# Performance work log

Hardware: AMD Instinct MI355X
Metric: run time of the kernel (lower is better)

The kernel has to match this reference:

```python
import jax, jax.numpy as jnp
import numpy as np


def conv1d_same(x, w, b, dilation=1):
    # x: [B, T, Cin], w: [K, Cin, Cout] (WIO), 'same' padding, stride 1
    y = jax.lax.conv_general_dilated(
        x, w, window_strides=(1,), padding='SAME',
        rhs_dilation=(dilation,), dimension_numbers=('NWC', 'WIO', 'NWC'))
    return y + b


def setup_inputs() -> dict:
    key = jax.random.key(0)
    ks = jax.random.split(key, 6)
    B, T, N_IN, N_OUT, ATTN_DIM, KSZ = 16, 2048, 96, 128, 64, 3
    return {
        'x': jax.random.normal(ks[0], (B, T, N_IN), jnp.float32),
        'qkv_w': jax.random.normal(ks[1], (N_IN, 3 * ATTN_DIM), jnp.float32) * 0.05,
        'qkv_b': jnp.zeros((3 * ATTN_DIM,), jnp.float32),
        'scale': jnp.ones((), jnp.float32),
        'conv_w1': jax.random.normal(ks[2], (KSZ, ATTN_DIM, N_OUT), jnp.float32) * 0.05,
        'conv_b1': jnp.zeros((N_OUT,), jnp.float32),
        'conv_w2': jax.random.normal(ks[3], (KSZ, N_OUT, N_OUT), jnp.float32) * 0.05,
        'conv_b2': jnp.zeros((N_OUT,), jnp.float32),
        'down_w': jax.random.normal(ks[4], (N_IN, N_OUT), jnp.float32) * 0.1,
    }


def reference(x, qkv_w, qkv_b, scale, conv_w1, conv_b1, conv_w2, conv_b2, down_w):
    # Dense4Attention: single Dense(3*attn_dim), split into q,k,v
    qkv = x @ qkv_w + qkv_b                       # [B,T,3*D]
    q, k, v = jnp.split(qkv, 3, axis=-1)          # each [B,T,D]
    # AttentionBlock: scores = q k^T * learned scale; non-causal (default)
    scores = jnp.einsum('btd,bsd->bts', q, k) * scale   # [B,T,T]
    weights = jax.nn.softmax(scores, axis=2)            # softmax_axis=2
    out_attn = jnp.einsum('bts,bsd->btd', weights, v)   # [B,T,D]
    h = jax.nn.relu(conv1d_same(out_attn, conv_w1, conv_b1, 1))
    out = jax.nn.relu(conv1d_same(h, conv_w2, conv_b2, 1))   # [B,T,n_out]
    # enhanced residual: softmax over time of row-sums of attn weights
    weight_x = jax.nn.softmax(jnp.sum(weights, axis=2), axis=1)  # [B,T]
    en_res_x = (weight_x[..., None] * x) @ down_w   # n_in != n_out -> downsample
    res = x @ down_w                                 # skip path downsample
    return jax.nn.relu(out + res + en_res_x)
```

## Files before the change

kernel.cpp:

```cpp
#include <hip/hip_runtime.h>
#include <cstdint>

#define B_   16
#define T_   2048
#define CIN  96
#define DH   64
#define NOUT 128

typedef float floatx4 __attribute__((ext_vector_type(4)));
typedef short shortx8 __attribute__((ext_vector_type(8)));
typedef unsigned int uintx2 __attribute__((ext_vector_type(2)));

__device__ __forceinline__ unsigned short f2bf(float f) {
  unsigned int u = __float_as_uint(f);
  u += 0x7FFFu + ((u >> 16) & 1u);
  return (unsigned short)(u >> 16);
}
__device__ __forceinline__ floatx4 f4zero() { floatx4 v; v[0]=0.f;v[1]=0.f;v[2]=0.f;v[3]=0.f; return v; }
__device__ __forceinline__ shortx8 s8zero() { shortx8 v;
#pragma unroll
  for (int i=0;i<8;++i) v[i]=0; return v; }

__device__ __forceinline__ void plane_swap(uint32_t& a, uint32_t& b) {
#if __has_builtin(__builtin_amdgcn_permlane32_swap) && __has_builtin(__builtin_amdgcn_permlane16_swap)
  uintx2 r1 = __builtin_amdgcn_permlane32_swap(a, b, false, false);
  uintx2 r2 = __builtin_amdgcn_permlane16_swap(r1[0], r1[1], false, false);
  a = r2[0]; b = r2[1];
#else
  asm volatile("v_permlane32_swap_b32 %0, %1\n\t"
               "v_permlane16_swap_b32 %0, %1"
               : "+v"(a), "+v"(b));
#endif
}

__global__ __launch_bounds__(256) void k_wprep(
    const float* __restrict__ qkv_w, const float* __restrict__ cw1,
    const float* __restrict__ cw2, const float* __restrict__ dw,
    unsigned short* __restrict__ qwt, unsigned short* __restrict__ w1t,
    unsigned short* __restrict__ w2t, unsigned short* __restrict__ dwt)
{
  int o = blockIdx.x * 256 + threadIdx.x;
  if (o < 18432) {
    int co = o / 96, ci = o % 96;
    qwt[o] = f2bf(qkv_w[ci * 192 + co]);
  } else if (o < 43008) {
    int p = o - 18432;
    int tap = p / 8192, rem = p % 8192, co = rem >> 6, ci = rem & 63;
    w1t[p] = f2bf(cw1[(tap * 64 + ci) * 128 + co]);
  } else if (o < 92160) {
    int p = o - 43008;
    int tap = p / 16384, rem = p % 16384, co = rem >> 7, ci = rem & 127;
    w2t[p] = f2bf(cw2[(tap * 128 + ci) * 128 + co]);
  } else if (o < 104448) {
    int p = o - 92160;
    int co = p / 96, ci = p % 96;
    dwt[p] = f2bf(dw[ci * 128 + co]);
  }
}

__global__ __launch_bounds__(256) void k_qkv(
    const float* __restrict__ x, const unsigned short* __restrict__ qwt,
    const float* __restrict__ qkv_b, const float* __restrict__ scale_p,
    unsigned short* __restrict__ qb, unsigned short* __restrict__ kb,
    unsigned short* __restrict__ vT)
{
  __shared__ __align__(16) unsigned short Xs[64][104];
  const int bx = blockIdx.x;
  const int b = bx >> 5, t0 = (bx & 31) * 64;
  const int tid = threadIdx.x, wave = tid >> 6, lane = tid & 63;
  const int l15 = lane & 15, quad = lane >> 4;
  const float scl2 = scale_p[0] * 1.4426950408889634f;

  for (int idx = tid; idx < 64 * 24; idx += 256) {
    int r = idx / 24, c = (idx % 24) * 4;
    float4 xv = *(const float4*)(x + ((size_t)(b * T_ + t0 + r)) * CIN + c);
    ushort4 o; o.x = f2bf(xv.x); o.y = f2bf(xv.y); o.z = f2bf(xv.z); o.w = f2bf(xv.w);
    *(ushort4*)(&Xs[r][c]) = o;
  }
  __syncthreads();

  floatx4 acc[4][3];
#pragma unroll
  for (int mt = 0; mt < 4; ++mt)
#pragma unroll
    for (int nt = 0; nt < 3; ++nt) acc[mt][nt] = f4zero();

#pragma unroll
  for (int ks = 0; ks < 3; ++ks) {
    shortx8 wf[3];
#pragma unroll
    for (int nt = 0; nt < 3; ++nt) {
      int j = wave * 48 + nt * 16 + l15;
      wf[nt] = *(const shortx8*)(qwt + (size_t)j * 96 + ks * 32 + quad * 8);
    }
#pragma unroll
    for (int mt = 0; mt < 4; ++mt) {
      shortx8 af = *(const shortx8*)(&Xs[mt * 16 + l15][ks * 32 + quad * 8]);
#pragma unroll
      for (int nt = 0; nt < 3; ++nt)
        acc[mt][nt] = __builtin_amdgcn_mfma_f32_16x16x32_bf16(af, wf[nt], acc[mt][nt], 0, 0, 0);
    }
  }

#pragma unroll
  for (int nt = 0; nt < 3; ++nt) {
    int j0 = wave * 48 + nt * 16;
    int j = j0 + l15;
    float bias = qkv_b[j];
#pragma unroll
    for (int mt = 0; mt < 4; ++mt) {
#pragma unroll
      for (int r = 0; r < 4; ++r) {
        int t = t0 + mt * 16 + quad * 4 + r;
        float v = acc[mt][nt][r] + bias;
        if (j0 < 64)        qb[((size_t)b * T_ + t) * DH + j] = f2bf(v * scl2);
        else if (j0 < 128)  kb[((size_t)b * T_ + t) * DH + (j - 64)] = f2bf(v);
        else                vT[((size_t)b * DH + (j - 128)) * T_ + t] = f2bf(v);
      }
    }
  }
}

__global__ __launch_bounds__(256) void k_attn(
    const unsigned short* __restrict__ qb, const unsigned short* __restrict__ kb,
    const unsigned short* __restrict__ vT,
    float* __restrict__ opart, float* __restrict__ lws)
{
  __shared__ __align__(16) unsigned short Kt[64][72];
  __shared__ __align__(16) unsigned short Vt[80][72];
  const int bx = blockIdx.x;
  const int half = bx & 1, qt = (bx >> 1) & 31, b = bx >> 6;
  const int tid = threadIdx.x, wave = tid >> 6, lane = tid & 63;
  const int l15 = lane & 15, quad = lane >> 4;

  const unsigned short* qrow = qb + ((size_t)b * T_ + qt * 64 + wave * 16 + l15) * DH;
  shortx8 qf0 = *(const shortx8*)(qrow + quad * 8);
  shortx8 qf1 = *(const shortx8*)(qrow + 32 + quad * 8);

  floatx4 O[5];
#pragma unroll
  for (int i = 0; i < 5; ++i) O[i] = f4zero();

  const unsigned short* kbase = kb + (size_t)b * T_ * DH + (size_t)half * 1024 * DH;
  const unsigned short* vbase = vT + (size_t)b * DH * T_ + half * 1024;

  for (int idx = tid; idx < 16 * 72; idx += 256) {
    int r = idx / 72, c = idx % 72;
    Vt[64 + r][c] = (r == 0) ? (unsigned short)0x3F80 : (unsigned short)0;
  }

  const int kr0 = tid >> 3, kc = (tid & 7) * 8;
  shortx8 pk[2], pv[2];
#pragma unroll
  for (int i = 0; i < 2; ++i) {
    pk[i] = *(const shortx8*)(kbase + (size_t)(kr0 + i * 32) * DH + kc);
    pv[i] = *(const shortx8*)(vbase + (size_t)(kr0 + i * 32) * T_ + kc);
  }

  for (int t = 0; t < 16; ++t) {
#pragma unroll
    for (int i = 0; i < 2; ++i) {
      *(shortx8*)(&Kt[kr0 + i * 32][kc]) = pk[i];
      *(shortx8*)(&Vt[kr0 + i * 32][kc]) = pv[i];
    }
    __syncthreads();

    if (t < 15) {
      int s0 = (t + 1) * 64;
#pragma unroll
      for (int i = 0; i < 2; ++i) {
        pk[i] = *(const shortx8*)(kbase + (size_t)(s0 + kr0 + i * 32) * DH + kc);
        pv[i] = *(const shortx8*)(vbase + (size_t)(kr0 + i * 32) * T_ + s0 + kc);
      }
    }

    floatx4 S[4];
#pragma unroll
    for (int nt = 0; nt < 4; ++nt) {
      shortx8 bk0 = *(const shortx8*)(&Kt[nt * 16 + l15][quad * 8]);
      shortx8 bk1 = *(const shortx8*)(&Kt[nt * 16 + l15][32 + quad * 8]);
      S[nt] = f4zero();
      S[nt] = __builtin_amdgcn_mfma_f32_16x16x32_bf16(bk0, qf0, S[nt], 0, 0, 0);
      S[nt] = __builtin_amdgcn_mfma_f32_16x16x32_bf16(bk1, qf1, S[nt], 0, 0, 0);
    }

    uint32_t pkv[8];
#pragma unroll
    for (int nt = 0; nt < 4; ++nt) {
#pragma unroll
      for (int j = 0; j < 2; ++j) {
        float lo = exp2f(S[nt][2 * j]);
        float hi = exp2f(S[nt][2 * j + 1]);
        pkv[nt * 2 + j] = (uint32_t)f2bf(lo) | ((uint32_t)f2bf(hi) << 16);
      }
    }

#pragma unroll
    for (int kk = 0; kk < 2; ++kk) {
      uint32_t a0 = pkv[4 * kk + 0], b0 = pkv[4 * kk + 2];
      plane_swap(a0, b0);
      uint32_t a1 = pkv[4 * kk + 1], b1 = pkv[4 * kk + 3];
      plane_swap(a1, b1);
      union { shortx8 s; uint32_t u[4]; } fu;
      fu.u[0] = a0; fu.u[1] = a1; fu.u[2] = b0; fu.u[3] = b1;
#pragma unroll
      for (int dt = 0; dt < 5; ++dt) {
        shortx8 bv = *(const shortx8*)(&Vt[dt * 16 + l15][kk * 32 + quad * 8]);
        O[dt] = __builtin_amdgcn_mfma_f32_16x16x32_bf16(fu.s, bv, O[dt], 0, 0, 0);
      }
    }
    __syncthreads();
  }

  float* obase = opart + (((size_t)(half * B_ + b) * T_) + qt * 64 + wave * 16) * DH;
#pragma unroll
  for (int r = 0; r < 4; ++r) {
    int row = quad * 4 + r;
#pragma unroll
    for (int dt = 0; dt < 4; ++dt)
      obase[(size_t)row * DH + dt * 16 + l15] = O[dt][r];
    if (l15 == 0)
      lws[half * (B_ * T_) + b * T_ + qt * 64 + wave * 16 + row] = O[4][r];
  }
}

__global__ __launch_bounds__(256) void k_comb(
    const float* __restrict__ opart, const float* __restrict__ lws,
    unsigned short* __restrict__ ab)
{
  int g = blockIdx.x * 256 + threadIdx.x;
  int bt = g >> 4, dg = (g & 15) * 4;
  const size_t HS = (size_t)B_ * T_ * DH;
  float4 p0 = *(const float4*)(opart + (size_t)bt * DH + dg);
  float4 p1 = *(const float4*)(opart + HS + (size_t)bt * DH + dg);
  float inv = 1.f / (lws[bt] + lws[B_ * T_ + bt]);
  ushort4 o;
  o.x = f2bf((p0.x + p1.x) * inv);
  o.y = f2bf((p0.y + p1.y) * inv);
  o.z = f2bf((p0.z + p1.z) * inv);
  o.w = f2bf((p0.w + p1.w) * inv);
  *(ushort4*)(ab + (size_t)bt * DH + dg) = o;
}

__global__ __launch_bounds__(256) void k_conv1(
    const unsigned short* __restrict__ ab, const unsigned short* __restrict__ w1t,
    const float* __restrict__ b1, unsigned short* __restrict__ hb)
{
  __shared__ __align__(16) unsigned short At[66][72];
  const int bx = blockIdx.x;
  const int b = bx >> 5, t0 = (bx & 31) * 64;
  const int tid = threadIdx.x, wave = tid >> 6, lane = tid & 63;
  const int l15 = lane & 15, quad = lane >> 4;

  for (int idx = tid; idx < 66 * 8; idx += 256) {
    int r = idx >> 3, c = (idx & 7) * 8;
    int t = t0 + r - 1;
    shortx8 v = s8zero();
    if (t >= 0 && t < T_) v = *(const shortx8*)(ab + ((size_t)b * T_ + t) * DH + c);
    *(shortx8*)(&At[r][c]) = v;
  }
  __syncthreads();

  floatx4 acc[4][2];
#pragma unroll
  for (int mt = 0; mt < 4; ++mt) { acc[mt][0] = f4zero(); acc[mt][1] = f4zero(); }

#pragma unroll
  for (int tap = 0; tap < 3; ++tap) {
#pragma unroll
    for (int ks = 0; ks < 2; ++ks) {
      shortx8 wf[2];
#pragma unroll
      for (int ct = 0; ct < 2; ++ct) {
        int co = wave * 32 + ct * 16 + l15;
        wf[ct] = *(const shortx8*)(w1t + ((size_t)tap * 128 + co) * 64 + ks * 32 + quad * 8);
      }
#pragma unroll
      for (int mt = 0; mt < 4; ++mt) {
        shortx8 af = *(const shortx8*)(&At[mt * 16 + l15 + tap][ks * 32 + quad * 8]);
        acc[mt][0] = __builtin_amdgcn_mfma_f32_16x16x32_bf16(af, wf[0], acc[mt][0], 0, 0, 0);
        acc[mt][1] = __builtin_amdgcn_mfma_f32_16x16x32_bf16(af, wf[1], acc[mt][1], 0, 0, 0);
      }
    }
  }

#pragma unroll
  for (int ct = 0; ct < 2; ++ct) {
    int co = wave * 32 + ct * 16 + l15;
    float bias = b1[co];
#pragma unroll
    for (int mt = 0; mt < 4; ++mt)
#pragma unroll
      for (int r = 0; r < 4; ++r) {
        int t = t0 + mt * 16 + quad * 4 + r;
        hb[((size_t)b * T_ + t) * NOUT + co] = f2bf(fmaxf(acc[mt][ct][r] + bias, 0.f));
      }
  }
}

__global__ __launch_bounds__(256) void k_conv2(
    const unsigned short* __restrict__ hb, const float* __restrict__ x,
    const unsigned short* __restrict__ w2t, const unsigned short* __restrict__ dwt,
    const float* __restrict__ b2, float* __restrict__ out)
{
  __shared__ __align__(16) unsigned short Ht[66][136];
  __shared__ __align__(16) unsigned short Xt[64][104];
  const int bx = blockIdx.x;
  const int b = bx >> 5, t0 = (bx & 31) * 64;
  const int tid = threadIdx.x, wave = tid >> 6, lane = tid & 63;
  const int l15 = lane & 15, quad = lane >> 4;

  for (int idx = tid; idx < 66 * 16; idx += 256) {
    int r = idx >> 4, c = (idx & 15) * 8;
    int t = t0 + r - 1;
    shortx8 v = s8zero();
    if (t >= 0 && t < T_) v = *(const shortx8*)(hb + ((size_t)b * T_ + t) * NOUT + c);
    *(shortx8*)(&Ht[r][c]) = v;
  }
  for (int idx = tid; idx < 64 * 24; idx += 256) {
    int r = idx / 24, c = (idx % 24) * 4;
    float4 xv = *(const float4*)(x + ((size_t)(b * T_ + t0 + r)) * CIN + c);
    ushort4 o; o.x = f2bf(xv.x); o.y = f2bf(xv.y); o.z = f2bf(xv.z); o.w = f2bf(xv.w);
    *(ushort4*)(&Xt[r][c]) = o;
  }
  __syncthreads();

  floatx4 a2[4][2], ar[4][2];
#pragma unroll
  for (int mt = 0; mt < 4; ++mt) { a2[mt][0]=f4zero(); a2[mt][1]=f4zero(); ar[mt][0]=f4zero(); ar[mt][1]=f4zero(); }

#pragma unroll
  for (int tap = 0; tap < 3; ++tap) {
#pragma unroll
    for (int ks = 0; ks < 4; ++ks) {
      shortx8 wf[2];
#pragma unroll
      for (int ct = 0; ct < 2; ++ct) {
        int co = wave * 32 + ct * 16 + l15;
        wf[ct] = *(const shortx8*)(w2t + ((size_t)tap * 128 + co) * 128 + ks * 32 + quad * 8);
      }
#pragma unroll
      for (int mt = 0; mt < 4; ++mt) {
        shortx8 af = *(const shortx8*)(&Ht[mt * 16 + l15 + tap][ks * 32 + quad * 8]);
        a2[mt][0] = __builtin_amdgcn_mfma_f32_16x16x32_bf16(af, wf[0], a2[mt][0], 0, 0, 0);
        a2[mt][1] = __builtin_amdgcn_mfma_f32_16x16x32_bf16(af, wf[1], a2[mt][1], 0, 0, 0);
      }
    }
  }
#pragma unroll
  for (int ks = 0; ks < 3; ++ks) {
    shortx8 wf[2];
#pragma unroll
    for (int ct = 0; ct < 2; ++ct) {
      int co = wave * 32 + ct * 16 + l15;
      wf[ct] = *(const shortx8*)(dwt + (size_t)co * 96 + ks * 32 + quad * 8);
    }
#pragma unroll
    for (int mt = 0; mt < 4; ++mt) {
      shortx8 af = *(const shortx8*)(&Xt[mt * 16 + l15][ks * 32 + quad * 8]);
      ar[mt][0] = __builtin_amdgcn_mfma_f32_16x16x32_bf16(af, wf[0], ar[mt][0], 0, 0, 0);
      ar[mt][1] = __builtin_amdgcn_mfma_f32_16x16x32_bf16(af, wf[1], ar[mt][1], 0, 0, 0);
    }
  }

  const float kres = 1.0f + 1.0f / 2048.0f;
#pragma unroll
  for (int ct = 0; ct < 2; ++ct) {
    int co = wave * 32 + ct * 16 + l15;
    float bias = b2[co];
#pragma unroll
    for (int mt = 0; mt < 4; ++mt)
#pragma unroll
      for (int r = 0; r < 4; ++r) {
        int t = t0 + mt * 16 + quad * 4 + r;
        float o2 = fmaxf(a2[mt][ct][r] + bias, 0.f);
        out[((size_t)b * T_ + t) * NOUT + co] = fmaxf(o2 + ar[mt][ct][r] * kres, 0.f);
      }
  }
}

extern "C" void kernel_launch(void* const* d_in, const int* in_sizes, int n_in,
                              void* d_out, int out_size, void* d_ws, size_t ws_size,
                              hipStream_t stream) {
  const float* x      = (const float*)d_in[0];
  const float* qkv_w  = (const float*)d_in[1];
  const float* qkv_b  = (const float*)d_in[2];
  const float* scale  = (const float*)d_in[3];
  const float* cw1    = (const float*)d_in[4];
  const float* cb1    = (const float*)d_in[5];
  const float* cw2    = (const float*)d_in[6];
  const float* cb2    = (const float*)d_in[7];
  const float* dw     = (const float*)d_in[8];

  char* ws = (char*)d_ws;
  unsigned short* qb  = (unsigned short*)(ws + 0);
  unsigned short* kb  = (unsigned short*)(ws + 4194304);
  unsigned short* vT  = (unsigned short*)(ws + 8388608);
  unsigned short* ab  = (unsigned short*)(ws + 12582912);
  unsigned short* hb  = (unsigned short*)(ws + 16777216);
  unsigned short* qwt = (unsigned short*)(ws + 25165824);
  unsigned short* w1t = (unsigned short*)(ws + 25202688);
  unsigned short* w2t = (unsigned short*)(ws + 25251840);
  unsigned short* dwt = (unsigned short*)(ws + 25350144);
  float*          lws = (float*)(ws + 25374720);

  float* opart = (float*)d_out;

  k_wprep<<<408, 256, 0, stream>>>(qkv_w, cw1, cw2, dw, qwt, w1t, w2t, dwt);
  k_qkv  <<<512, 256, 0, stream>>>(x, qwt, qkv_b, scale, qb, kb, vT);
  k_attn <<<1024, 256, 0, stream>>>(qb, kb, vT, opart, lws);
  k_comb <<<2048, 256, 0, stream>>>(opart, lws, ab);
  k_conv1<<<512, 256, 0, stream>>>(ab, w1t, cb1, hb);
  k_conv2<<<512, 256, 0, stream>>>(hb, x, w2t, dwt, cb2, (float*)d_out);
}
```

Measured before the change: 152.1 us.

## Drop split-KV in attention and fuse normalization into kernel epilogue

The attention kernel no longer splits the key range into two halves. Each block now loops over all 2048 keys and normalizes its output by the accumulated row sum before writing bf16 directly. This removes the separate combine kernel and the fp32 partial-output and row-sum round trip through global memory. The trade-off is half as many blocks (512), each running twice as long, which lowers parallelism. The softmax P packing also switches from manual bf16 rounding to the hardware v_cvt_pk_bf16_f32 instruction.

```diff
diff --git a/kernel.cpp b/kernel.cpp
--- a/kernel.cpp
+++ b/kernel.cpp
@@ -15,6 +15,11 @@
   unsigned int u = __float_as_uint(f);
   u += 0x7FFFu + ((u >> 16) & 1u);
   return (unsigned short)(u >> 16);
+}
+__device__ __forceinline__ uint32_t cvtpk(float lo, float hi) {
+  uint32_t r;
+  asm("v_cvt_pk_bf16_f32 %0, %1, %2" : "=v"(r) : "v"(lo), "v"(hi));
+  return r;
 }
 __device__ __forceinline__ floatx4 f4zero() { floatx4 v; v[0]=0.f;v[1]=0.f;v[2]=0.f;v[3]=0.f; return v; }
 __device__ __forceinline__ shortx8 s8zero() { shortx8 v;
@@ -124,12 +129,12 @@
 __global__ __launch_bounds__(256) void k_attn(
     const unsigned short* __restrict__ qb, const unsigned short* __restrict__ kb,
     const unsigned short* __restrict__ vT,
-    float* __restrict__ opart, float* __restrict__ lws)
+    unsigned short* __restrict__ ab)
 {
   __shared__ __align__(16) unsigned short Kt[64][72];
   __shared__ __align__(16) unsigned short Vt[80][72];
   const int bx = blockIdx.x;
-  const int half = bx & 1, qt = (bx >> 1) & 31, b = bx >> 6;
+  const int qt = bx & 31, b = bx >> 5;
   const int tid = threadIdx.x, wave = tid >> 6, lane = tid & 63;
   const int l15 = lane & 15, quad = lane >> 4;
 
@@ -141,8 +146,8 @@
 #pragma unroll
   for (int i = 0; i < 5; ++i) O[i] = f4zero();
 
-  const unsigned short* kbase = kb + (size_t)b * T_ * DH + (size_t)half * 1024 * DH;
-  const unsigned short* vbase = vT + (size_t)b * DH * T_ + half * 1024;
+  const unsigned short* kbase = kb + (size_t)b * T_ * DH;
+  const unsigned short* vbase = vT + (size_t)b * DH * T_;
 
   for (int idx = tid; idx < 16 * 72; idx += 256) {
     int r = idx / 72, c = idx % 72;
@@ -157,7 +162,7 @@
     pv[i] = *(const shortx8*)(vbase + (size_t)(kr0 + i * 32) * T_ + kc);
   }
 
-  for (int t = 0; t < 16; ++t) {
+  for (int t = 0; t < 32; ++t) {
 #pragma unroll
     for (int i = 0; i < 2; ++i) {
       *(shortx8*)(&Kt[kr0 + i * 32][kc]) = pk[i];
@@ -165,7 +170,7 @@
     }
     __syncthreads();
 
-    if (t < 15) {
+    if (t < 31) {
       int s0 = (t + 1) * 64;
 #pragma unroll
       for (int i = 0; i < 2; ++i) {
@@ -188,11 +193,8 @@
 #pragma unroll
     for (int nt = 0; nt < 4; ++nt) {
 #pragma unroll
-      for (int j = 0; j < 2; ++j) {
-        float lo = exp2f(S[nt][2 * j]);
-        float hi = exp2f(S[nt][2 * j + 1]);
-        pkv[nt * 2 + j] = (uint32_t)f2bf(lo) | ((uint32_t)f2bf(hi) << 16);
-      }
+      for (int j = 0; j < 2; ++j)
+        pkv[nt * 2 + j] = cvtpk(exp2f(S[nt][2 * j]), exp2f(S[nt][2 * j + 1]));
     }
 
 #pragma unroll
@@ -212,34 +214,16 @@
     __syncthreads();
   }
 
-  float* obase = opart + (((size_t)(half * B_ + b) * T_) + qt * 64 + wave * 16) * DH;
+  unsigned short* abase = ab + ((size_t)b * T_ + qt * 64 + wave * 16) * DH;
 #pragma unroll
   for (int r = 0; r < 4; ++r) {
+    float s = __shfl(O[4][r], quad << 4);
+    float inv = 1.f / s;
     int row = quad * 4 + r;
 #pragma unroll
     for (int dt = 0; dt < 4; ++dt)
-      obase[(size_t)row * DH + dt * 16 + l15] = O[dt][r];
-    if (l15 == 0)
-      lws[half * (B_ * T_) + b * T_ + qt * 64 + wave * 16 + row] = O[4][r];
-  }
-}
-
-__global__ __launch_bounds__(256) void k_comb(
-    const float* __restrict__ opart, const float* __restrict__ lws,
-    unsigned short* __restrict__ ab)
-{
-  int g = blockIdx.x * 256 + threadIdx.x;
-  int bt = g >> 4, dg = (g & 15) * 4;
-  const size_t HS = (size_t)B_ * T_ * DH;
-  float4 p0 = *(const float4*)(opart + (size_t)bt * DH + dg);
-  float4 p1 = *(const float4*)(opart + HS + (size_t)bt * DH + dg);
-  float inv = 1.f / (lws[bt] + lws[B_ * T_ + bt]);
-  ushort4 o;
-  o.x = f2bf((p0.x + p1.x) * inv);
-  o.y = f2bf((p0.y + p1.y) * inv);
-  o.z = f2bf((p0.z + p1.z) * inv);
-  o.w = f2bf((p0.w + p1.w) * inv);
-  *(ushort4*)(ab + (size_t)bt * DH + dg) = o;
+      abase[(size_t)row * DH + dt * 16 + l15] = f2bf(O[dt][r] * inv);
+  }
 }
 
 __global__ __launch_bounds__(256) void k_conv1(
@@ -402,14 +386,10 @@
   unsigned short* w1t = (unsigned short*)(ws + 25202688);
   unsigned short* w2t = (unsigned short*)(ws + 25251840);
   unsigned short* dwt = (unsigned short*)(ws + 25350144);
-  float*          lws = (float*)(ws + 25374720);
-
-  float* opart = (float*)d_out;
 
   k_wprep<<<408, 256, 0, stream>>>(qkv_w, cw1, cw2, dw, qwt, w1t, w2t, dwt);
   k_qkv  <<<512, 256, 0, stream>>>(x, qwt, qkv_b, scale, qb, kb, vT);
-  k_attn <<<1024, 256, 0, stream>>>(qb, kb, vT, opart, lws);
-  k_comb <<<2048, 256, 0, stream>>>(opart, lws, ab);
+  k_attn <<<512, 256, 0, stream>>>(qb, kb, vT, ab);
   k_conv1<<<512, 256, 0, stream>>>(ab, w1t, cb1, hb);
   k_conv2<<<512, 256, 0, stream>>>(hb, x, w2t, dwt, cb2, (float*)d_out);
 }
```

Result: faster. 146.7 us (-3.5%).
